# Kernel tuning notes

Hardware: AMD Instinct MI355X
Metric: run time of the kernel (lower is better)

The kernel has to match this reference:

```python
import jax, jax.numpy as jnp
import numpy as np

B, S, D = 2, 2048, 1024
H, E = 16, 64          # n_heads, head_dim
DFF = 4096             # intermediate
R_ATTN, R_OUT, R_FF = 32, 512, 512
LN_EPS = 1e-5
SCALE = 1.0 / np.sqrt(E)


def setup_inputs() -> dict:
    key = jax.random.key(0)
    ks = jax.random.split(key, 24)
    s = 0.02
    inp = {
        "hidden_states": jax.random.normal(ks[0], (B, S, D), jnp.float32),
        "ln1_w": jnp.ones((D,), jnp.float32),
        "ln1_b": jnp.zeros((D,), jnp.float32),
        "q_U": jax.random.normal(ks[1], (H, E, R_ATTN), jnp.float32) * s,
        "q_V": jax.random.normal(ks[2], (H, R_ATTN, D), jnp.float32) * s,
        "q_bias": jax.random.normal(ks[3], (H, E), jnp.float32) * s,
        "k_U": jax.random.normal(ks[4], (H, E, R_ATTN), jnp.float32) * s,
        "k_V": jax.random.normal(ks[5], (H, R_ATTN, D), jnp.float32) * s,
        "k_bias": jax.random.normal(ks[6], (H, E), jnp.float32) * s,
        "v_U": jax.random.normal(ks[7], (H, E, R_ATTN), jnp.float32) * s,
        "v_V": jax.random.normal(ks[8], (H, R_ATTN, D), jnp.float32) * s,
        "v_bias": jax.random.normal(ks[9], (H, E), jnp.float32) * s,
        "out_U": jax.random.normal(ks[10], (D, R_OUT), jnp.float32) * s,
        "out_V": jax.random.normal(ks[11], (R_OUT, D), jnp.float32) * s,
        "out_bias": jnp.zeros((D,), jnp.float32),
        "ln2_w": jnp.ones((D,), jnp.float32),
        "ln2_b": jnp.zeros((D,), jnp.float32),
        "fc1_U": jax.random.normal(ks[12], (DFF, R_FF), jnp.float32) * s,
        "fc1_V": jax.random.normal(ks[13], (R_FF, D), jnp.float32) * s,
        "fc1_bias": jnp.zeros((DFF,), jnp.float32),
        "fc2_U": jax.random.normal(ks[14], (D, R_FF), jnp.float32) * s,
        "fc2_V": jax.random.normal(ks[15], (R_FF, DFF), jnp.float32) * s,
        "fc2_bias": jnp.zeros((D,), jnp.float32),
    }
    return inp


def _layernorm(x, w, b):
    mu = jnp.mean(x, axis=-1, keepdims=True)
    var = jnp.mean(jnp.square(x - mu), axis=-1, keepdims=True)
    return (x - mu) * jax.lax.rsqrt(var + LN_EPS) * w + b


def _per_head_svd(x, U, V, bias):
    # x: [b,s,d]; V: [h,r,d]; U: [h,e,r]; bias: [h,e] -> [b,h,s,e]
    t = jnp.einsum("bsd,hrd->bhsr", x, V)
    return jnp.einsum("bhsr,her->bhse", t, U) + bias[None, :, None, :]


def reference(hidden_states, ln1_w, ln1_b, q_U, q_V, q_bias, k_U, k_V, k_bias,
              v_U, v_V, v_bias, out_U, out_V, out_bias, ln2_w, ln2_b,
              fc1_U, fc1_V, fc1_bias, fc2_U, fc2_V, fc2_bias):
    b, s, d = hidden_states.shape
    normed = _layernorm(hidden_states, ln1_w, ln1_b)

    q = _per_head_svd(normed, q_U, q_V, q_bias)  # [b,h,s,e]
    k = _per_head_svd(normed, k_U, k_V, k_bias)
    v = _per_head_svd(normed, v_U, v_V, v_bias)

    scores = jnp.einsum("bhqe,bhke->bhqk", q, k) * SCALE
    causal = jnp.tril(jnp.ones((s, s), dtype=bool))
    scores = jnp.where(causal, scores, -jnp.inf)
    probs = jax.nn.softmax(scores, axis=-1)
    attn = jnp.einsum("bhqk,bhke->bhqe", probs, v)
    attn = attn.transpose(0, 2, 1, 3).reshape(b, s, d)  # [b,s,d]

    attn = jnp.einsum("bsr,dr->bsd", jnp.einsum("bsd,rd->bsr", attn, out_V), out_U) + out_bias
    hidden_states = hidden_states + attn

    normed = _layernorm(hidden_states, ln2_w, ln2_b)
    ff = jnp.einsum("bsr,fr->bsf", jnp.einsum("bsd,rd->bsr", normed, fc1_V), fc1_U) + fc1_bias
    ff = jax.nn.gelu(ff, approximate=False)  # exact erf gelu as in torch F.gelu
    ff = jnp.einsum("bsr,dr->bsd", jnp.einsum("bsf,rf->bsr", ff, fc2_V), fc2_U) + fc2_bias
    hidden_states = hidden_states + ff
    return (hidden_states,)
```

## Files before the change

### kernel.cpp

```cpp
#include <hip/hip_runtime.h>
#include <hip/hip_bf16.h>
#include <math.h>

#define Bc 2
#define Sc 2048
#define Dc 1024
#define Hc 16
#define Ec 64
#define DFFc 4096
#define SCALEc 0.125f
#define SCLOG2E 0.18033688f
#define LN_EPSc 1e-5f
#define BH_STRIDE 131072

typedef short bf16x8 __attribute__((ext_vector_type(8)));
typedef unsigned short u16x4 __attribute__((ext_vector_type(4)));
typedef unsigned short u16x8 __attribute__((ext_vector_type(8)));
typedef float f32x4 __attribute__((ext_vector_type(4)));
typedef float f32x16 __attribute__((ext_vector_type(16)));
typedef unsigned int u32x4 __attribute__((ext_vector_type(4)));
#define MFMA16(a, b, c) __builtin_amdgcn_mfma_f32_16x16x32_bf16(a, b, c, 0, 0, 0)
#define MFMA32(a, b, c) __builtin_amdgcn_mfma_f32_32x32x16_bf16(a, b, c, 0, 0, 0)
#define GLDS16(g, l)                                                            \
  __builtin_amdgcn_global_load_lds((const __attribute__((address_space(1))) void*)(g), \
                                   (__attribute__((address_space(3))) void*)(l), 16, 0, 0)

static __device__ __forceinline__ unsigned short f2bf(float x) {
  unsigned u = __float_as_uint(x);
  unsigned r = (u + 0x7FFFu + ((u >> 16) & 1u)) >> 16;
  return (unsigned short)r;
}
static __device__ __forceinline__ unsigned cvtpk(float lo, float hi) {
  unsigned r;
  asm("v_cvt_pk_bf16_f32 %0, %1, %2" : "=v"(r) : "v"(lo), "v"(hi));
  return r;
}

__global__ __launch_bounds__(256) void convert9(
    const float* __restrict__ s0, const float* __restrict__ s1, const float* __restrict__ s2,
    const float* __restrict__ s3, const float* __restrict__ s4, const float* __restrict__ s5,
    const float* __restrict__ s6, const float* __restrict__ s7, const float* __restrict__ s8,
    unsigned short* __restrict__ wsu) {
  int i = (blockIdx.x * 256 + threadIdx.x) * 4;
  const float* s;
  int off;
  if (i < 3145728) {
    int seg = i >> 19;
    off = i & 524287;
    s = (seg == 0) ? s0 : (seg == 1) ? s1 : (seg == 2) ? s2
        : (seg == 3) ? s3 : (seg == 4) ? s4 : s5;
  } else if (i < 5242880) { s = s6; off = i - 3145728; }
  else if (i < 7340032)   { s = s7; off = i - 5242880; }
  else if (i < 7864320)   { s = s8; off = i - 7340032; }
  else return;
  float4 v = *(const float4*)(s + off);
  u16x4 o = {f2bf(v.x), f2bf(v.y), f2bf(v.z), f2bf(v.w)};
  *(u16x4*)(wsu + i) = o;
}

__global__ __launch_bounds__(256) void ln_bf16(const float* __restrict__ x,
                                               const float* __restrict__ w,
                                               const float* __restrict__ b,
                                               unsigned short* __restrict__ out) {
  __shared__ float sm[8];
  int row = blockIdx.x;
  int tid = threadIdx.x;
  const float* xr = x + (size_t)row * Dc;
  float v[4];
  float sum = 0.f;
#pragma unroll
  for (int i = 0; i < 4; ++i) { v[i] = xr[tid + i * 256]; sum += v[i]; }
#pragma unroll
  for (int off = 32; off > 0; off >>= 1) sum += __shfl_down(sum, off, 64);
  if ((tid & 63) == 0) sm[tid >> 6] = sum;
  __syncthreads();
  float mean = (sm[0] + sm[1] + sm[2] + sm[3]) * (1.f / Dc);
  float var = 0.f;
#pragma unroll
  for (int i = 0; i < 4; ++i) { float d0 = v[i] - mean; var += d0 * d0; }
#pragma unroll
  for (int off = 32; off > 0; off >>= 1) var += __shfl_down(var, off, 64);
  if ((tid & 63) == 0) sm[4 + (tid >> 6)] = var;
  __syncthreads();
  float rstd = rsqrtf((sm[4] + sm[5] + sm[6] + sm[7]) * (1.f / Dc) + LN_EPSc);
  unsigned short* orow = out + (size_t)row * Dc;
#pragma unroll
  for (int i = 0; i < 4; ++i) {
    int c = tid + i * 256;
    orow[c] = f2bf((v[i] - mean) * rstd * w[c] + b[c]);
  }
}

template <int BM, int BN>
__global__ __launch_bounds__(256) void gemm_bf16(const unsigned short* __restrict__ A,
                                                 const unsigned short* __restrict__ W,
                                                 float* __restrict__ Cf,
                                                 unsigned short* __restrict__ Cb,
                                                 const float* __restrict__ bias,
                                                 const float* __restrict__ res,
                                                 int M, int N, int K, int gelu, int nbm) {
  constexpr int BK = 64;
  constexpr int MT = BM / 32;
  constexpr int NT = BN / 32;
  __shared__ unsigned short As[2][BM * BK];
  __shared__ unsigned short Bs[2][BN * BK];
  int tid = threadIdx.x;
  int lane = tid & 63;
  int wid = tid >> 6;
  int cl = lane & 15, grp = lane >> 4;
  int wr = wid >> 1, wc = wid & 1;
  int bm = blockIdx.x % nbm;
  int bn = blockIdx.x / nbm;
  const unsigned short* Ab = A + (size_t)(bm * BM) * K;
  const unsigned short* Wb = W + (size_t)(bn * BN) * K;
  f32x4 acc[MT][NT];
  f32x4 z4 = {0.f, 0.f, 0.f, 0.f};
#pragma unroll
  for (int i = 0; i < MT; ++i)
#pragma unroll
    for (int j = 0; j < NT; ++j) acc[i][j] = z4;
  int r0 = tid >> 3;
  int c0 = (tid & 7) * 8;

#define STAGE(buf, k0)                                                         \
  {                                                                            \
    _Pragma("unroll") for (int l = 0; l < BM / 32; ++l) {                      \
      int row = r0 + l * 32;                                                   \
      int sc = c0 ^ ((row & 7) * 8);                                           \
      GLDS16(Ab + (size_t)row * K + (k0) + sc, &As[buf][(tid + l * 256) * 8]); \
    }                                                                          \
    _Pragma("unroll") for (int l = 0; l < BN / 32; ++l) {                      \
      int row = r0 + l * 32;                                                   \
      int sc = c0 ^ ((row & 7) * 8);                                           \
      GLDS16(Wb + (size_t)row * K + (k0) + sc, &Bs[buf][(tid + l * 256) * 8]); \
    }                                                                          \
  }

  int nt = K / BK;
  STAGE(0, 0)
  __syncthreads();
  for (int t = 0; t < nt; ++t) {
    int cur = t & 1;
    if (t + 1 < nt) STAGE(cur ^ 1, (t + 1) * BK)
#pragma unroll
    for (int kk = 0; kk < 2; ++kk) {
      bf16x8 af[MT], bfr[NT];
#pragma unroll
      for (int i = 0; i < MT; ++i) {
        int row = wr * (BM / 2) + i * 16 + cl;
        af[i] = *(const bf16x8*)&As[cur][row * BK + ((kk * 32 + grp * 8) ^ ((row & 7) * 8))];
      }
#pragma unroll
      for (int j = 0; j < NT; ++j) {
        int row = wc * (BN / 2) + j * 16 + cl;
        bfr[j] = *(const bf16x8*)&Bs[cur][row * BK + ((kk * 32 + grp * 8) ^ ((row & 7) * 8))];
      }
#pragma unroll
      for (int i = 0; i < MT; ++i)
#pragma unroll
        for (int j = 0; j < NT; ++j) acc[i][j] = MFMA16(af[i], bfr[j], acc[i][j]);
    }
    __syncthreads();
  }
#undef STAGE

#pragma unroll
  for (int i = 0; i < MT; ++i) {
    int row = bm * BM + wr * (BM / 2) + i * 16 + grp * 4;
#pragma unroll
    for (int j = 0; j < NT; ++j) {
      int col = bn * BN + wc * (BN / 2) + j * 16 + cl;
      float bv = bias ? bias[col] : 0.f;
#pragma unroll
      for (int r = 0; r < 4; ++r) {
        float v = acc[i][j][r] + bv;
        if (gelu) v = 0.5f * v * (1.f + erff(v * 0.70710678118f));
        if (res) v += res[(size_t)(row + r) * N + col];
        if (Cb) Cb[(size_t)(row + r) * N + col] = f2bf(v);
        else Cf[(size_t)(row + r) * N + col] = v;
      }
    }
  }
}

__global__ __launch_bounds__(256) void expand_all(const float* __restrict__ t,
                                                  const float* __restrict__ qU,
                                                  const float* __restrict__ kU,
                                                  const float* __restrict__ vU,
                                                  const float* __restrict__ qB,
                                                  const float* __restrict__ kB,
                                                  const float* __restrict__ vB,
                                                  unsigned short* __restrict__ qO,
                                                  unsigned short* __restrict__ kO,
                                                  unsigned short* __restrict__ vO) {
  __shared__ float Us[64][33];
  __shared__ float Ts[32][33];
  int blk = blockIdx.x;
  int kind = blk >> 11;
  int inner = blk & 2047;
  int sb = inner & 63;
  int h = (inner >> 6) & 15;
  int b = inner >> 10;
  int bh = b * Hc + h;
  int tid = threadIdx.x;
  const float* U = (kind == 0) ? qU : (kind == 1) ? kU : vU;
  const float* bias = (kind == 0) ? qB : (kind == 1) ? kB : vB;
  int toff = kind * 512;
  for (int i = tid; i < 64 * 32; i += 256) Us[i >> 5][i & 31] = U[h * 2048 + i];
  for (int i = tid; i < 32 * 32; i += 256) {
    int sr = i >> 5, r = i & 31;
    Ts[sr][r] = t[(size_t)(b * Sc + sb * 32 + sr) * 1536 + toff + h * 32 + r];
  }
  __syncthreads();
  if (kind < 2) {
    unsigned short* out = (kind == 0) ? qO : kO;
    float prescale = (kind == 0) ? SCLOG2E : 1.0f;
    int s = tid >> 3;
    int ec = tid & 7;
    float acc[8];
#pragma unroll
    for (int j = 0; j < 8; ++j) acc[j] = bias[h * 64 + ec * 8 + j];
    for (int r = 0; r < 32; ++r) {
      float tv = Ts[s][r];
#pragma unroll
      for (int j = 0; j < 8; ++j) acc[j] += tv * Us[ec * 8 + j][r];
    }
    u16x8 v8;
#pragma unroll
    for (int j = 0; j < 8; ++j) v8[j] = f2bf(acc[j] * prescale);
    int es = ec >> 1, hi = ec & 1;
    int lane = s + hi * 32;
    *(u16x8*)(out + (size_t)bh * BH_STRIDE + (size_t)(((sb * 4 + es) * 64 + lane)) * 8) = v8;
  } else {
    int e = tid & 63;
    int sg = tid >> 6;
    float bv = bias[h * 64 + e];
    u16x8 v8;
#pragma unroll
    for (int si = 0; si < 8; ++si) {
      int sr = sg * 8 + si;
      float acc = bv;
#pragma unroll
      for (int r = 0; r < 32; ++r) acc += Ts[sr][r] * Us[e][r];
      v8[si] = f2bf(acc);
    }
    int eo = e >> 5, ll = e & 31;
    int h2 = sg >> 1, hi = sg & 1;
    int ix = eo * 2 + h2;
    int lane = ll + hi * 32;
    *(u16x8*)(vO + (size_t)bh * BH_STRIDE + (size_t)(((sb * 4 + ix) * 64 + lane)) * 8) = v8;
  }
}

__global__ __launch_bounds__(256) void attn_mfma(const unsigned short* __restrict__ qf_,
                                                 const unsigned short* __restrict__ kf_,
                                                 const unsigned short* __restrict__ vf_,
                                                 unsigned short* __restrict__ out) {
  __shared__ float MS[2][34][64];
  int tid = threadIdx.x;
  int wid = tid >> 6;
  int lane = tid & 63;
  int ll = lane & 31;
  int hi = lane >> 5;
  int bid = blockIdx.x;
  int xcd = bid & 7;
  int idx = bid >> 3;
  int qt = 63 - (idx >> 2);
  int bh = xcd + 8 * (idx & 3);
  int b = bh >> 4, h = bh & 15;
  const unsigned short* qb = qf_ + (size_t)bh * BH_STRIDE;
  const unsigned short* kb = kf_ + (size_t)bh * BH_STRIDE;
  const unsigned short* vb = vf_ + (size_t)bh * BH_STRIDE;
  int q0 = qt * 32;
  int nt = qt + 1;
  int full = nt - 1;
  int fs = wid * full / 4;
  int fe = (wid + 1) * full / 4;

  bf16x8 qf[4];
#pragma unroll
  for (int es = 0; es < 4; ++es)
    qf[es] = *(const bf16x8*)(qb + (size_t)((qt * 4 + es) * 64 + lane) * 8);

  f32x16 accO[2] = {};
  float m = -1e30f, l = 0.f;

  int t = fs;
  for (; t + 1 < fe; t += 2) {
    bf16x8 ka[4], kb2[4];
#pragma unroll
    for (int es = 0; es < 4; ++es) {
      ka[es] = *(const bf16x8*)(kb + (size_t)((t * 4 + es) * 64 + lane) * 8);
      kb2[es] = *(const bf16x8*)(kb + (size_t)(((t + 1) * 4 + es) * 64 + lane) * 8);
    }
    f32x16 cA = {}, cB = {};
    __builtin_amdgcn_s_setprio(1);
    cA = MFMA32(ka[0], qf[0], cA);
    cA = MFMA32(ka[1], qf[1], cA);
    cA = MFMA32(ka[2], qf[2], cA);
    cA = MFMA32(ka[3], qf[3], cA);
    cB = MFMA32(kb2[0], qf[0], cB);
    cB = MFMA32(kb2[1], qf[1], cB);
    cB = MFMA32(kb2[2], qf[2], cB);
    cB = MFMA32(kb2[3], qf[3], cB);
    __builtin_amdgcn_s_setprio(0);
    float s[32];
#pragma unroll
    for (int r = 0; r < 16; ++r) { s[r] = cA[r]; s[16 + r] = cB[r]; }
    float mx[16];
#pragma unroll
    for (int r = 0; r < 16; ++r) mx[r] = fmaxf(s[r], s[16 + r]);
#pragma unroll
    for (int st = 8; st > 0; st >>= 1)
#pragma unroll
      for (int r = 0; r < 8; ++r)
        if (r < st) mx[r] = fmaxf(mx[r], mx[r + st]);
    float tmax = fmaxf(mx[0], __shfl_xor(mx[0], 32, 64));
    if (!__all(tmax <= m)) {
      float mn = fmaxf(m, tmax);
      float corr = exp2f(m - mn);
      m = mn;
      l *= corr;
#pragma unroll
      for (int r = 0; r < 16; ++r) { accO[0][r] *= corr; accO[1][r] *= corr; }
    }
#pragma unroll
    for (int r = 0; r < 32; ++r) s[r] = exp2f(s[r] - m);
#pragma unroll
    for (int r = 0; r < 16; ++r) mx[r] = s[r] + s[16 + r];
#pragma unroll
    for (int st = 8; st > 0; st >>= 1)
#pragma unroll
      for (int r = 0; r < 8; ++r)
        if (r < st) mx[r] += mx[r + st];
    l += mx[0];
    bf16x8 va[4], vb2[4];
#pragma unroll
    for (int ix = 0; ix < 4; ++ix) {
      va[ix] = *(const bf16x8*)(vb + (size_t)((t * 4 + ix) * 64 + lane) * 8);
      vb2[ix] = *(const bf16x8*)(vb + (size_t)(((t + 1) * 4 + ix) * 64 + lane) * 8);
    }
    unsigned wA0 = cvtpk(s[0], s[1]), wA1 = cvtpk(s[2], s[3]);
    unsigned wA2 = cvtpk(s[4], s[5]), wA3 = cvtpk(s[6], s[7]);
    unsigned wA4 = cvtpk(s[8], s[9]), wA5 = cvtpk(s[10], s[11]);
    unsigned wA6 = cvtpk(s[12], s[13]), wA7 = cvtpk(s[14], s[15]);
    unsigned wB0 = cvtpk(s[16], s[17]), wB1 = cvtpk(s[18], s[19]);
    unsigned wB2 = cvtpk(s[20], s[21]), wB3 = cvtpk(s[22], s[23]);
    unsigned wB4 = cvtpk(s[24], s[25]), wB5 = cvtpk(s[26], s[27]);
    unsigned wB6 = cvtpk(s[28], s[29]), wB7 = cvtpk(s[30], s[31]);
    asm("v_permlane32_swap_b32 %0, %1" : "+v"(wA0), "+v"(wA2));
    asm("v_permlane32_swap_b32 %0, %1" : "+v"(wA1), "+v"(wA3));
    asm("v_permlane32_swap_b32 %0, %1" : "+v"(wA4), "+v"(wA6));
    asm("v_permlane32_swap_b32 %0, %1" : "+v"(wA5), "+v"(wA7));
    asm("v_permlane32_swap_b32 %0, %1" : "+v"(wB0), "+v"(wB2));
    asm("v_permlane32_swap_b32 %0, %1" : "+v"(wB1), "+v"(wB3));
    asm("v_permlane32_swap_b32 %0, %1" : "+v"(wB4), "+v"(wB6));
    asm("v_permlane32_swap_b32 %0, %1" : "+v"(wB5), "+v"(wB7));
    u32x4 pA0 = {wA0, wA1, wA2, wA3}, pA1 = {wA4, wA5, wA6, wA7};
    u32x4 pB0 = {wB0, wB1, wB2, wB3}, pB1 = {wB4, wB5, wB6, wB7};
    bf16x8 bA0 = __builtin_bit_cast(bf16x8, pA0), bA1 = __builtin_bit_cast(bf16x8, pA1);
    bf16x8 bB0 = __builtin_bit_cast(bf16x8, pB0), bB1 = __builtin_bit_cast(bf16x8, pB1);
    __builtin_amdgcn_s_setprio(1);
    accO[0] = MFMA32(va[0], bA0, accO[0]);
    accO[0] = MFMA32(va[1], bA1, accO[0]);
    accO[0] = MFMA32(vb2[0], bB0, accO[0]);
    accO[0] = MFMA32(vb2[1], bB1, accO[0]);
    accO[1] = MFMA32(va[2], bA0, accO[1]);
    accO[1] = MFMA32(va[3], bA1, accO[1]);
    accO[1] = MFMA32(vb2[2], bB0, accO[1]);
    accO[1] = MFMA32(vb2[3], bB1, accO[1]);
    __builtin_amdgcn_s_setprio(0);
  }

#define ATT_ONE(T, MASKED)                                                          \
  {                                                                                 \
    bf16x8 kf1[4];                                                                  \
    _Pragma("unroll") for (int es = 0; es < 4; ++es)                                \
      kf1[es] = *(const bf16x8*)(kb + (size_t)(((T) * 4 + es) * 64 + lane) * 8);    \
    f32x16 c = {};                                                                  \
    __builtin_amdgcn_s_setprio(1);                                                  \
    c = MFMA32(kf1[0], qf[0], c);                                                   \
    c = MFMA32(kf1[1], qf[1], c);                                                   \
    c = MFMA32(kf1[2], qf[2], c);                                                   \
    c = MFMA32(kf1[3], qf[3], c);                                                   \
    __builtin_amdgcn_s_setprio(0);                                                  \
    float s1[16];                                                                   \
    _Pragma("unroll") for (int r = 0; r < 16; ++r) {                                \
      s1[r] = c[r];                                                                 \
      if (MASKED) {                                                                 \
        int keyloc = (r & 3) + 8 * (r >> 2) + 4 * hi;                               \
        if (keyloc > ll) s1[r] = -1e30f;                                            \
      }                                                                             \
    }                                                                               \
    float u0 = fmaxf(fmaxf(fmaxf(s1[0], s1[1]), fmaxf(s1[2], s1[3])),               \
                     fmaxf(fmaxf(s1[4], s1[5]), fmaxf(s1[6], s1[7])));              \
    float u1 = fmaxf(fmaxf(fmaxf(s1[8], s1[9]), fmaxf(s1[10], s1[11])),             \
                     fmaxf(fmaxf(s1[12], s1[13]), fmaxf(s1[14], s1[15])));          \
    float tmax = fmaxf(u0, u1);                                                     \
    tmax = fmaxf(tmax, __shfl_xor(tmax, 32, 64));                                   \
    if (!__all(tmax <= m)) {                                                        \
      float mn = fmaxf(m, tmax);                                                    \
      float corr = exp2f(m - mn);                                                   \
      m = mn;                                                                       \
      l *= corr;                                                                    \
      _Pragma("unroll") for (int r = 0; r < 16; ++r) {                              \
        accO[0][r] *= corr; accO[1][r] *= corr;                                     \
      }                                                                             \
    }                                                                               \
    float lp = 0.f;                                                                 \
    _Pragma("unroll") for (int r = 0; r < 16; ++r) { s1[r] = exp2f(s1[r] - m); lp += s1[r]; } \
    l += lp;                                                                        \
    bf16x8 vf1[4];                                                                  \
    _Pragma("unroll") for (int ix = 0; ix < 4; ++ix)                                \
      vf1[ix] = *(const bf16x8*)(vb + (size_t)(((T) * 4 + ix) * 64 + lane) * 8);    \
    unsigned w0 = cvtpk(s1[0], s1[1]), w1 = cvtpk(s1[2], s1[3]);                    \
    unsigned w2 = cvtpk(s1[4], s1[5]), w3 = cvtpk(s1[6], s1[7]);                    \
    unsigned w4 = cvtpk(s1[8], s1[9]), w5 = cvtpk(s1[10], s1[11]);                  \
    unsigned w6 = cvtpk(s1[12], s1[13]), w7 = cvtpk(s1[14], s1[15]);                \
    asm("v_permlane32_swap_b32 %0, %1" : "+v"(w0), "+v"(w2));                       \
    asm("v_permlane32_swap_b32 %0, %1" : "+v"(w1), "+v"(w3));                       \
    asm("v_permlane32_swap_b32 %0, %1" : "+v"(w4), "+v"(w6));                       \
    asm("v_permlane32_swap_b32 %0, %1" : "+v"(w5), "+v"(w7));                       \
    u32x4 pw0 = {w0, w1, w2, w3};                                                   \
    u32x4 pw1 = {w4, w5, w6, w7};                                                   \
    bf16x8 pb0 = __builtin_bit_cast(bf16x8, pw0);                                   \
    bf16x8 pb1 = __builtin_bit_cast(bf16x8, pw1);                                   \
    __builtin_amdgcn_s_setprio(1);                                                  \
    accO[0] = MFMA32(vf1[0], pb0, accO[0]);                                         \
    accO[0] = MFMA32(vf1[1], pb1, accO[0]);                                         \
    accO[1] = MFMA32(vf1[2], pb0, accO[1]);                                         \
    accO[1] = MFMA32(vf1[3], pb1, accO[1]);                                         \
    __builtin_amdgcn_s_setprio(0);                                                  \
  }

  if (t < fe) ATT_ONE(t, false)
  if (wid == 3) ATT_ONE(full, true)
#undef ATT_ONE

  auto publish = [&](int slot) {
#pragma unroll
    for (int r = 0; r < 16; ++r) {
      MS[slot][r][lane] = accO[0][r];
      MS[slot][16 + r][lane] = accO[1][r];
    }
    MS[slot][32][lane] = m;
    MS[slot][33][lane] = l;
  };
  auto merge = [&](int slot) {
    float mw = MS[slot][32][lane];
    float lw = MS[slot][33][lane];
    float ms = fmaxf(m, mw);
    float sc = exp2f(m - ms);
    float sw = exp2f(mw - ms);
    m = ms;
    l = l * sc + lw * sw;
#pragma unroll
    for (int r = 0; r < 16; ++r) {
      accO[0][r] = accO[0][r] * sc + MS[slot][r][lane] * sw;
      accO[1][r] = accO[1][r] * sc + MS[slot][16 + r][lane] * sw;
    }
  };
  if (wid == 1) publish(0);
  if (wid == 3) publish(1);
  __syncthreads();
  if (wid == 0) merge(0);
  if (wid == 2) merge(1);
  __syncthreads();
  if (wid == 2) publish(0);
  __syncthreads();
  if (wid == 0) {
    merge(0);
    float ltot = l + __shfl_xor(l, 32, 64);
    float inv = 1.f / ltot;
    unsigned short* orow = out + (size_t)(b * Sc + q0 + ll) * Dc + h * Ec;
#pragma unroll
    for (int eo = 0; eo < 2; ++eo)
#pragma unroll
      for (int r = 0; r < 16; ++r) {
        int e = eo * 32 + (r & 3) + 8 * (r >> 2) + 4 * hi;
        orow[e] = f2bf(accO[eo][r] * inv);
      }
  }
}

extern "C" void kernel_launch(void* const* d_in, const int* in_sizes, int n_in,
                              void* d_out, int out_size, void* d_ws, size_t ws_size,
                              hipStream_t stream) {
  const float* hidden = (const float*)d_in[0];
  const float* ln1_w = (const float*)d_in[1];
  const float* ln1_b = (const float*)d_in[2];
  const float* q_U = (const float*)d_in[3];
  const float* q_V = (const float*)d_in[4];
  const float* q_bias = (const float*)d_in[5];
  const float* k_U = (const float*)d_in[6];
  const float* k_V = (const float*)d_in[7];
  const float* k_bias = (const float*)d_in[8];
  const float* v_U = (const float*)d_in[9];
  const float* v_V = (const float*)d_in[10];
  const float* v_bias = (const float*)d_in[11];
  const float* out_U = (const float*)d_in[12];
  const float* out_V = (const float*)d_in[13];
  const float* out_bias = (const float*)d_in[14];
  const float* ln2_w = (const float*)d_in[15];
  const float* ln2_b = (const float*)d_in[16];
  const float* fc1_U = (const float*)d_in[17];
  const float* fc1_V = (const float*)d_in[18];
  const float* fc1_bias = (const float*)d_in[19];
  const float* fc2_U = (const float*)d_in[20];
  const float* fc2_V = (const float*)d_in[21];
  const float* fc2_bias = (const float*)d_in[22];
  float* out = (float*)d_out;
  float* ws = (float*)d_ws;
  unsigned short* wsu = (unsigned short*)d_ws;

  unsigned short* wQKV = wsu;
  unsigned short* wOUTV = wsu + 1572864;
  unsigned short* wOUTU = wsu + 2097152;
  unsigned short* wFC1V = wsu + 2621440;
  unsigned short* wFC1U = wsu + 3145728;
  unsigned short* wFC2V = wsu + 5242880;
  unsigned short* wFC2U = wsu + 7340032;

  float* h1 = ws + 4194304;
  unsigned short* attn_out = (unsigned short*)(ws + 6291456);
  unsigned short* normed = (unsigned short*)(ws + 8388608);
  float* rb = ws + 10485760;
  unsigned short* rbB = (unsigned short*)(ws + 10485760);
  unsigned short* ff = (unsigned short*)(ws + 11534336);
  unsigned short* qbuf = (unsigned short*)(ws + 16777216);
  unsigned short* kbuf = (unsigned short*)(ws + 18874368);
  unsigned short* rbG = (unsigned short*)(ws + 19922944);
  unsigned short* vtbuf = (unsigned short*)(ws + 20971520);

  const int M = Bc * Sc;
  dim3 blk(256);

  convert9<<<7680, blk, 0, stream>>>(q_V, k_V, v_V, out_V, out_U, fc1_V, fc1_U, fc2_V, fc2_U, wsu);

  ln_bf16<<<M, blk, 0, stream>>>(hidden, ln1_w, ln1_b, normed);

  gemm_bf16<64, 64><<<1536, blk, 0, stream>>>(normed, wQKV, rb, nullptr, nullptr, nullptr,
                                              M, 1536, Dc, 0, 64);
  expand_all<<<6144, blk, 0, stream>>>(rb, q_U, k_U, v_U, q_bias, k_bias, v_bias,
                                       qbuf, kbuf, vtbuf);

  attn_mfma<<<2048, blk, 0, stream>>>(qbuf, kbuf, vtbuf, attn_out);

  gemm_bf16<64, 64><<<512, blk, 0, stream>>>(attn_out, wOUTV, nullptr, rbB, nullptr, nullptr,
                                             M, 512, Dc, 0, 64);
  gemm_bf16<64, 64><<<1024, blk, 0, stream>>>(rbB, wOUTU, h1, nullptr, out_bias, hidden,
                                              M, Dc, 512, 0, 64);

  ln_bf16<<<M, blk, 0, stream>>>(h1, ln2_w, ln2_b, normed);
  gemm_bf16<64, 64><<<512, blk, 0, stream>>>(normed, wFC1V, nullptr, rbB, nullptr, nullptr,
                                             M, 512, Dc, 0, 64);
  gemm_bf16<128, 64><<<2048, blk, 0, stream>>>(rbB, wFC1U, nullptr, ff, fc1_bias, nullptr,
                                               M, DFFc, 512, 1, 32);
  gemm_bf16<64, 64><<<512, blk, 0, stream>>>(ff, wFC2V, nullptr, rbG, nullptr, nullptr,
                                             M, 512, DFFc, 0, 64);
  gemm_bf16<64, 64><<<1024, blk, 0, stream>>>(rbG, wFC2U, out, nullptr, fc2_bias, h1,
                                              M, Dc, 512, 0, 64);
}
```

Measured before the change: 274.9 us.

## Restructure GEMM main loop with fine-grained vmcnt waits and split LDS-read/MFMA phases

The bf16 GEMM loop drops the end-of-iteration __syncthreads. It now issues the next tile's global-to-LDS loads, then waits with a partial s_waitcnt vmcnt so only the current tile's loads must finish before a raw s_barrier. All LDS fragments for both k-halves are read into registers first, followed by an lgkmcnt wait and a barrier. The MFMA block then runs under raised wave priority via s_setprio. The goal is to let next-tile loads stay in flight during compute and to group MFMAs densely, at the cost of more live fragment registers and hand-coded waitcnt values tied to the load count per stage.

```diff
diff --git a/kernel.cpp b/kernel.cpp
--- a/kernel.cpp
+++ b/kernel.cpp
@@ -102,6 +102,7 @@
   constexpr int BK = 64;
   constexpr int MT = BM / 32;
   constexpr int NT = BN / 32;
+  constexpr int NLD = BM / 32 + BN / 32;
   __shared__ unsigned short As[2][BM * BK];
   __shared__ unsigned short Bs[2][BN * BK];
   int tid = threadIdx.x;
@@ -138,29 +139,46 @@
 
   int nt = K / BK;
   STAGE(0, 0)
-  __syncthreads();
+  asm volatile("s_waitcnt vmcnt(0)" ::: "memory");
+  __builtin_amdgcn_s_barrier();
   for (int t = 0; t < nt; ++t) {
     int cur = t & 1;
-    if (t + 1 < nt) STAGE(cur ^ 1, (t + 1) * BK)
+    if (t + 1 < nt) {
+      STAGE(cur ^ 1, (t + 1) * BK)
+      if constexpr (NLD == 4) asm volatile("s_waitcnt vmcnt(4)" ::: "memory");
+      else if constexpr (NLD == 6) asm volatile("s_waitcnt vmcnt(6)" ::: "memory");
+      else asm volatile("s_waitcnt vmcnt(0)" ::: "memory");
+      __builtin_amdgcn_s_barrier();
+    }
+    if (t + 1 == nt && nt > 1) {
+      asm volatile("s_waitcnt vmcnt(0)" ::: "memory");
+      __builtin_amdgcn_s_barrier();
+    }
+    bf16x8 af[2][MT], bfr[2][NT];
 #pragma unroll
     for (int kk = 0; kk < 2; ++kk) {
-      bf16x8 af[MT], bfr[NT];
 #pragma unroll
       for (int i = 0; i < MT; ++i) {
         int row = wr * (BM / 2) + i * 16 + cl;
-        af[i] = *(const bf16x8*)&As[cur][row * BK + ((kk * 32 + grp * 8) ^ ((row & 7) * 8))];
+        af[kk][i] = *(const bf16x8*)&As[cur][row * BK + ((kk * 32 + grp * 8) ^ ((row & 7) * 8))];
       }
 #pragma unroll
       for (int j = 0; j < NT; ++j) {
         int row = wc * (BN / 2) + j * 16 + cl;
-        bfr[j] = *(const bf16x8*)&Bs[cur][row * BK + ((kk * 32 + grp * 8) ^ ((row & 7) * 8))];
+        bfr[kk][j] = *(const bf16x8*)&Bs[cur][row * BK + ((kk * 32 + grp * 8) ^ ((row & 7) * 8))];
       }
+    }
+    asm volatile("s_waitcnt lgkmcnt(0)" ::: "memory");
+    __builtin_amdgcn_sched_barrier(0);
+    __builtin_amdgcn_s_barrier();
+    __builtin_amdgcn_s_setprio(1);
+#pragma unroll
+    for (int kk = 0; kk < 2; ++kk)
 #pragma unroll
       for (int i = 0; i < MT; ++i)
 #pragma unroll
-        for (int j = 0; j < NT; ++j) acc[i][j] = MFMA16(af[i], bfr[j], acc[i][j]);
-    }
-    __syncthreads();
+        for (int j = 0; j < NT; ++j) acc[i][j] = MFMA16(af[kk][i], bfr[kk][j], acc[i][j]);
+    __builtin_amdgcn_s_setprio(0);
   }
 #undef STAGE
 
```

Result: no change. 277.4 us (+0.9%).
